# Kernel optimization log

Hardware: AMD Instinct MI355X
Metric: run time of the kernel (lower is better)

The kernel has to match this reference:

```python
import jax, jax.numpy as jnp
import numpy as np

N0, N1, N2, N3, B = 120000, 20000, 6000, 1600, 64
E1, E2, E3 = 480000, 144000, 38400
KS = 5  # kernel size per dim; K = 125 total


def spline_basis(pseudo, ks=KS):
    # open B-spline basis, degree 1, over [0,1]^3 (torch_spline_conv semantics)
    p = pseudo * (ks - 1)                       # (E,3)
    lo = jnp.clip(jnp.floor(p), 0.0, ks - 2.0)  # (E,3)
    f = p - lo                                  # fractional part
    bits = jnp.array([[(s >> d) & 1 for d in range(3)] for s in range(8)],
                     dtype=jnp.float32)         # (8,3) corner offsets
    w = jnp.where(bits[None] > 0, f[:, None, :], 1.0 - f[:, None, :])  # (E,8,3)
    basis = w[..., 0] * w[..., 1] * w[..., 2]   # (E,8)
    strides = jnp.array([1.0, ks, ks * ks], dtype=jnp.float32)
    kidx = ((lo[:, None, :] + bits[None]) * strides).sum(-1).astype(jnp.int32)  # (E,8)
    return basis, kidx


def spline_conv(x, edge_index, pseudo, W, root, bias, num_nodes):
    src, dst = edge_index[0], edge_index[1]
    basis, kidx = spline_basis(pseudo)                   # (E,8), (E,8)
    XW = jnp.einsum('ni,kio->nko', x, W)                 # (N,K,out)
    taps = XW[src[:, None], kidx]                        # (E,8,out) gather
    msg = (taps * basis[..., None]).sum(axis=1)          # (E,out)
    agg = jax.ops.segment_sum(msg, dst, num_segments=num_nodes)
    deg = jax.ops.segment_sum(jnp.ones_like(dst, jnp.float32), dst,
                              num_segments=num_nodes)
    agg = agg / jnp.maximum(deg, 1.0)[:, None]           # mean aggregation
    return agg + x @ root + bias


def seg_max(x, seg, n):
    v = jax.ops.segment_max(x, seg, num_segments=n)
    return jnp.where(jnp.isfinite(v), v, 0.0)  # empty voxels -> 0


def setup_inputs() -> dict:
    key = jax.random.key(0)
    ks = jax.random.split(key, 24)
    return {
        'x0': jax.random.uniform(ks[0], (N0, 1), jnp.float32),
        'cluster0': jax.random.randint(ks[1], (N0,), 0, N1),
        'edge1': jax.random.randint(ks[2], (2, E1), 0, N1),
        'pseudo1': jax.random.uniform(ks[3], (E1, 3), jnp.float32),
        'W1': jax.random.normal(ks[4], (125, 1, 64), jnp.float32) * 0.1,
        'root1': jax.random.normal(ks[5], (1, 64), jnp.float32) * 0.1,
        'b1': jnp.zeros((64,), jnp.float32),
        'cluster1': jax.random.randint(ks[6], (N1,), 0, N2),
        'edge2': jax.random.randint(ks[7], (2, E2), 0, N2),
        'pseudo2': jax.random.uniform(ks[8], (E2, 3), jnp.float32),
        'W2': jax.random.normal(ks[9], (125, 64, 64), jnp.float32) * 0.05,
        'root2': jax.random.normal(ks[10], (64, 64), jnp.float32) * 0.05,
        'b2': jnp.zeros((64,), jnp.float32),
        'cluster2': jax.random.randint(ks[11], (N2,), 0, N3),
        'edge3': jax.random.randint(ks[12], (2, E3), 0, N3),
        'pseudo3': jax.random.uniform(ks[13], (E3, 3), jnp.float32),
        'W3': jax.random.normal(ks[14], (125, 64, 128), jnp.float32) * 0.05,
        'root3': jax.random.normal(ks[15], (64, 128), jnp.float32) * 0.05,
        'b3': jnp.zeros((128,), jnp.float32),
        'cluster3': jax.random.randint(ks[16], (N3,), 0, B * 8),
        'fc1_w': jax.random.normal(ks[17], (1024, 256), jnp.float32) * 0.03,
        'fc1_b': jnp.zeros((256,), jnp.float32),
        'fc2_w': jax.random.normal(ks[18], (256, 10), jnp.float32) * 0.06,
        'fc2_b': jnp.zeros((10,), jnp.float32),
    }


def reference(x0, cluster0, edge1, pseudo1, W1, root1, b1,
              cluster1, edge2, pseudo2, W2, root2, b2,
              cluster2, edge3, pseudo3, W3, root3, b3,
              cluster3, fc1_w, fc1_b, fc2_w, fc2_b):
    x = seg_max(x0, cluster0, N1)                       # sparse voxel max pool 1
    x = jax.nn.elu(spline_conv(x, edge1, pseudo1, W1, root1, b1, N1))
    x = seg_max(x, cluster1, N2)                        # pool 2
    x = jax.nn.elu(spline_conv(x, edge2, pseudo2, W2, root2, b2, N2))
    x = seg_max(x, cluster2, N3)                        # pool 3
    x = jax.nn.elu(spline_conv(x, edge3, pseudo3, W3, root3, b3, N3))
    x = seg_max(x, cluster3, B * 8)                     # dense 2x2x2 voxel pool
    x = x.reshape(B, 8 * 128)
    x = jax.nn.elu(x @ fc1_w + fc1_b)
    x = x @ fc2_w + fc2_b
    return jax.nn.log_softmax(x, axis=1)
```

## Files before the change

kernel.cpp:

```cpp
#include <hip/hip_runtime.h>
#include <hip/hip_bf16.h>
#include <math.h>

#define N0c 120000
#define N1c 20000
#define N2c 6000
#define N3c 1600
#define E1c 480000
#define E2c 144000
#define E3c 38400

#define HB1 32
#define HB2 120
#define HB3 40
#define CVT2B 2000
#define CVT3B 4000
#define SS0B  469

typedef __attribute__((ext_vector_type(8))) short short8;
typedef __attribute__((ext_vector_type(4))) float f32x4;

__device__ __forceinline__ float eluf(float x) {
    return x > 0.0f ? x : expm1f(x);
}

__device__ __forceinline__ unsigned f2sort(float f) {
    unsigned u = __float_as_uint(f);
    return (u & 0x80000000u) ? ~u : (u | 0x80000000u);
}
__device__ __forceinline__ float sort2f(unsigned u) {
    unsigned bits = (u & 0x80000000u) ? (u & 0x7FFFFFFFu) : ~u;
    return __uint_as_float(bits);
}
__device__ __forceinline__ unsigned short f2bf(float v) {
    unsigned u = __float_as_uint(v);
    unsigned r = (u + 0x7FFFu + ((u >> 16) & 1u)) >> 16;
    return (unsigned short)r;
}

__global__ __launch_bounds__(256) void hist_all(
    const int* __restrict__ edge1, const int* __restrict__ edge2,
    const int* __restrict__ edge3,
    const float* __restrict__ pseudo2, const float* __restrict__ pseudo3,
    const float* __restrict__ W2, const float* __restrict__ W3,
    const float* __restrict__ x0, const int* __restrict__ cluster0,
    int* __restrict__ blockCnt1,
    int* __restrict__ blockCnt2, int* __restrict__ cntD2,
    int* __restrict__ blockCnt3, int* __restrict__ cntD3,
    unsigned short* __restrict__ W2t, unsigned short* __restrict__ W3t,
    unsigned* __restrict__ xm1)
{
    __shared__ int h[1250];
    int b = blockIdx.x, t = threadIdx.x;
    if (b < HB1) {
        for (int i = t; i < 1250; i += 256) h[i] = 0;
        __syncthreads();
        for (int e = b * 256 + t; e < E1c; e += HB1 * 256)
            atomicAdd(&h[edge1[E1c + e] >> 4], 1);
        __syncthreads();
        for (int i = t; i < 1250; i += 256) blockCnt1[i * HB1 + b] = h[i];
    } else if (b < HB1 + HB2 + HB3) {
        bool is2 = b < HB1 + HB2;
        int rb = is2 ? (b - HB1) : (b - HB1 - HB2);
        int nblk = is2 ? HB2 : HB3;
        int E = is2 ? E2c : E3c;
        const int* edge = is2 ? edge2 : edge3;
        const float* pseudo = is2 ? pseudo2 : pseudo3;
        int* blockCnt = is2 ? blockCnt2 : blockCnt3;
        int* dstCnt = is2 ? cntD2 : cntD3;
        int nb = is2 ? HB2 : HB3;
        if (t < 64) h[t] = 0;
        __syncthreads();
        for (int e = rb * 256 + t; e < E; e += nblk * 256) {
            int c = 0, mul = 1;
            #pragma unroll
            for (int d = 0; d < 3; d++) {
                float p = pseudo[e * 3 + d] * 4.0f;
                float l = fminf(fmaxf(floorf(p), 0.0f), 3.0f);
                c += (int)l * mul;
                mul <<= 2;
            }
            atomicAdd(&h[c], 1);
            atomicAdd(&dstCnt[edge[E + e]], 1);
        }
        __syncthreads();
        if (t < 64) blockCnt[t * nb + rb] = h[t];
    } else if (b < HB1 + HB2 + HB3 + CVT2B) {
        int idx = (b - (HB1 + HB2 + HB3)) * 256 + t;
        if (idx < 125 * 64 * 64) {
            int ic = idx & 63, kn = idx >> 6;
            int n = kn & 63, k = kn >> 6;
            W2t[idx] = f2bf(W2[((size_t)k * 64 + ic) * 64 + n]);
        }
    } else if (b < HB1 + HB2 + HB3 + CVT2B + CVT3B) {
        int idx = (b - (HB1 + HB2 + HB3 + CVT2B)) * 256 + t;
        if (idx < 125 * 128 * 64) {
            int ic = idx & 63, kn = idx >> 6;
            int n = kn & 127, k = kn >> 7;
            W3t[idx] = f2bf(W3[((size_t)k * 64 + ic) * 128 + n]);
        }
    } else {
        int idx = (b - (HB1 + HB2 + HB3 + CVT2B + CVT3B)) * 256 + t;
        if (idx < N0c)
            atomicMax(&xm1[cluster0[idx]], f2sort(x0[idx]));
    }
}

__global__ __launch_bounds__(256) void plan_tot(
    const int* __restrict__ blockCnt1, int* __restrict__ start1,
    const int* __restrict__ blockCnt2, int* __restrict__ binCnt2,
    int* __restrict__ binStart2, int* __restrict__ blkPrefix2,
    int* __restrict__ chunkBin2, int* __restrict__ chunkOff2,
    const int* __restrict__ blockCnt3, int* __restrict__ binCnt3,
    int* __restrict__ binStart3, int* __restrict__ blkPrefix3,
    int* __restrict__ chunkBin3, int* __restrict__ chunkOff3,
    const int* __restrict__ cntD2, int* __restrict__ dstStart2,
    const int* __restrict__ cntD3, int* __restrict__ dstStart3)
{
    __shared__ int ps[256];
    __shared__ int ps64[64];
    int t = threadIdx.x;

    int loc[5];
    int s = 0;
    #pragma unroll
    for (int i = 0; i < 5; i++) {
        int bin = t * 5 + i;
        int v = 0;
        if (bin < 1250) {
            const int4* row = (const int4*)(blockCnt1 + (size_t)bin * HB1);
            #pragma unroll
            for (int j = 0; j < HB1 / 4; j++) {
                int4 q = row[j];
                v += q.x + q.y + q.z + q.w;
            }
        }
        loc[i] = v;
        s += v;
    }
    ps[t] = s;
    __syncthreads();
    for (int ofs = 1; ofs < 256; ofs <<= 1) {
        int add = (t >= ofs) ? ps[t - ofs] : 0;
        __syncthreads();
        ps[t] += add;
        __syncthreads();
    }
    int run = (t == 0) ? 0 : ps[t - 1];
    #pragma unroll
    for (int i = 0; i < 5; i++) {
        int bin = t * 5 + i;
        if (bin < 1250) {
            start1[bin] = run;
            run += loc[i];
        }
    }
    if (t == 255) start1[1250] = run;
    __syncthreads();

    if (t < 64) {
        int v = 0;
        const int4* row = (const int4*)(blockCnt2 + (size_t)t * HB2);
        for (int j = 0; j < HB2 / 4; j++) {
            int4 q = row[j];
            v += q.x + q.y + q.z + q.w;
        }
        binCnt2[t] = v;
        ps64[t] = v;
    }
    __syncthreads();
    if (t == 0) {
        int s2 = 0, p = 0;
        for (int c = 0; c < 64; c++) {
            int v = ps64[c];
            binStart2[c] = s2;
            blkPrefix2[c] = p;
            s2 += v;
            p += (v + 63) >> 6;
        }
        binStart2[64] = s2;
        blkPrefix2[64] = p;
    }
    __syncthreads();
    if (t < 64) {
        int nch = (binCnt2[t] + 63) >> 6;
        int base = blkPrefix2[t];
        for (int j = 0; j < nch; j++) {
            chunkBin2[base + j] = t;
            chunkOff2[base + j] = j;
        }
    }
    __syncthreads();

    if (t < 64) {
        int v = 0;
        const int4* row = (const int4*)(blockCnt3 + (size_t)t * HB3);
        for (int j = 0; j < HB3 / 4; j++) {
            int4 q = row[j];
            v += q.x + q.y + q.z + q.w;
        }
        binCnt3[t] = v;
        ps64[t] = v;
    }
    __syncthreads();
    if (t == 0) {
        int s3 = 0, p = 0;
        for (int c = 0; c < 64; c++) {
            int v = ps64[c];
            binStart3[c] = s3;
            blkPrefix3[c] = p;
            s3 += v;
            p += (v + 63) >> 6;
        }
        binStart3[64] = s3;
        blkPrefix3[64] = p;
    }
    __syncthreads();
    if (t < 64) {
        int nch = (binCnt3[t] + 63) >> 6;
        int base = blkPrefix3[t];
        for (int j = 0; j < nch; j++) {
            chunkBin3[base + j] = t;
            chunkOff3[base + j] = j;
        }
    }
    __syncthreads();

    {
        int locd[24];
        int sd = 0;
        #pragma unroll
        for (int i = 0; i < 24; i++) {
            int bin = t * 24 + i;
            int vv = (bin < N2c) ? cntD2[bin] : 0;
            locd[i] = vv;
            sd += vv;
        }
        ps[t] = sd;
        __syncthreads();
        for (int ofs = 1; ofs < 256; ofs <<= 1) {
            int add = (t >= ofs) ? ps[t - ofs] : 0;
            __syncthreads();
            ps[t] += add;
            __syncthreads();
        }
        int rund = (t == 0) ? 0 : ps[t - 1];
        #pragma unroll
        for (int i = 0; i < 24; i++) {
            int bin = t * 24 + i;
            if (bin < N2c) { dstStart2[bin] = rund; rund += locd[i]; }
        }
        if (t == 255) dstStart2[N2c] = ps[255];
    }
    __syncthreads();

    {
        int locd[7];
        int sd = 0;
        #pragma unroll
        for (int i = 0; i < 7; i++) {
            int bin = t * 7 + i;
            int vv = (bin < N3c) ? cntD3[bin] : 0;
            locd[i] = vv;
            sd += vv;
        }
        ps[t] = sd;
        __syncthreads();
        for (int ofs = 1; ofs < 256; ofs <<= 1) {
            int add = (t >= ofs) ? ps[t - ofs] : 0;
            __syncthreads();
            ps[t] += add;
            __syncthreads();
        }
        int rund = (t == 0) ? 0 : ps[t - 1];
        #pragma unroll
        for (int i = 0; i < 7; i++) {
            int bin = t * 7 + i;
            if (bin < N3c) { dstStart3[bin] = rund; rund += locd[i]; }
        }
        if (t == 255) dstStart3[N3c] = ps[255];
    }
}

__global__ __launch_bounds__(256) void off_all(
    const int* __restrict__ blockCnt1, const int* __restrict__ start1,
    int* __restrict__ blockOff1,
    const int* __restrict__ blockCnt2, const int* __restrict__ binStart2,
    int* __restrict__ blockOff2,
    const int* __restrict__ blockCnt3, const int* __restrict__ binStart3,
    int* __restrict__ blockOff3)
{
    int r = blockIdx.x * 256 + threadIdx.x;
    if (r < 1250) {
        int run = start1[r];
        const int* c = blockCnt1 + (size_t)r * HB1;
        int* o = blockOff1 + (size_t)r * HB1;
        #pragma unroll 4
        for (int b = 0; b < HB1; b++) { o[b] = run; run += c[b]; }
    } else if (r < 1250 + 64) {
        int bin = r - 1250;
        int run = binStart2[bin];
        const int* c = blockCnt2 + (size_t)bin * HB2;
        int* o = blockOff2 + (size_t)bin * HB2;
        #pragma unroll 4
        for (int b = 0; b < HB2; b++) { o[b] = run; run += c[b]; }
    } else if (r < 1250 + 128) {
        int bin = r - 1314;
        int run = binStart3[bin];
        const int* c = blockCnt3 + (size_t)bin * HB3;
        int* o = blockOff3 + (size_t)bin * HB3;
        #pragma unroll 4
        for (int b = 0; b < HB3; b++) { o[b] = run; run += c[b]; }
    }
}

__global__ __launch_bounds__(256) void scatter_all(
    const int* __restrict__ edge1, const float* __restrict__ pseudo1,
    const int* __restrict__ edge2, const float* __restrict__ pseudo2,
    const int* __restrict__ edge3, const float* __restrict__ pseudo3,
    const int* __restrict__ blockOff1, const int* __restrict__ blockOff2,
    const int* __restrict__ blockOff3,
    int4* __restrict__ rec1, int4* __restrict__ rec2, int4* __restrict__ rec3,
    unsigned* __restrict__ xm1,
    const int* __restrict__ dstStart2, const int* __restrict__ dstStart3,
    int* __restrict__ curD2, int* __restrict__ curD3,
    int* __restrict__ posList2, int* __restrict__ posList3)
{
    __shared__ int cur[1250];
    int b = blockIdx.x, t = threadIdx.x;
    if (b < HB1) {
        for (int i = t; i < 1250; i += 256) cur[i] = blockOff1[(size_t)i * HB1 + b];
        __syncthreads();
        for (int e = b * 256 + t; e < E1c; e += HB1 * 256) {
            int src = edge1[e], dst = edge1[E1c + e];
            float f[3];
            int kbase = 0, mul5 = 1;
            #pragma unroll
            for (int d = 0; d < 3; d++) {
                float pp = pseudo1[e * 3 + d] * 4.0f;
                float l = fminf(fmaxf(floorf(pp), 0.0f), 3.0f);
                f[d] = pp - l;
                kbase += (int)l * mul5;
                mul5 *= 5;
            }
            int p = atomicAdd(&cur[dst >> 4], 1);
            rec1[p] = make_int4(src | ((dst & 15) << 16) | (kbase << 20),
                                __float_as_int(f[0]), __float_as_int(f[1]),
                                __float_as_int(f[2]));
        }
    } else if (b < HB1 + HB2 + HB3) {
        bool is2 = b < HB1 + HB2;
        int rb = is2 ? (b - HB1) : (b - HB1 - HB2);
        int nblk = is2 ? HB2 : HB3;
        int E = is2 ? E2c : E3c;
        const int* edge = is2 ? edge2 : edge3;
        const float* pseudo = is2 ? pseudo2 : pseudo3;
        const int* blockOff = is2 ? blockOff2 : blockOff3;
        int4* rec = is2 ? rec2 : rec3;
        const int* dstStart = is2 ? dstStart2 : dstStart3;
        int* curD = is2 ? curD2 : curD3;
        int* posList = is2 ? posList2 : posList3;
        int nb = is2 ? HB2 : HB3;
        if (t < 64) cur[t] = blockOff[(size_t)t * nb + rb];
        __syncthreads();
        for (int e = rb * 256 + t; e < E; e += nblk * 256) {
            int src = edge[e], dst = edge[E + e];
            float f[3];
            int c = 0, mul = 1;
            #pragma unroll
            for (int d = 0; d < 3; d++) {
                float pp = pseudo[e * 3 + d] * 4.0f;
                float l = fminf(fmaxf(floorf(pp), 0.0f), 3.0f);
                f[d] = pp - l;
                c += (int)l * mul;
                mul <<= 2;
            }
            int p = atomicAdd(&cur[c], 1);
            rec[p] = make_int4(src | (dst << 16),
                               __float_as_int(f[0]), __float_as_int(f[1]),
                               __float_as_int(f[2]));
            int qd = dstStart[dst] + atomicAdd(&curD[dst], 1);
            posList[qd] = p;
        }
    } else {
        int idx = (b - (HB1 + HB2 + HB3)) * 256 + t;
        if (idx < N1c) {
            float f = sort2f(xm1[idx]);
            unsigned bb = __float_as_uint(f);
            if ((bb & 0x7F800000u) == 0x7F800000u) f = 0.0f;
            ((float*)xm1)[idx] = f;
        }
    }
}

__global__ __launch_bounds__(256) void conv1_block(
    const int4* __restrict__ rec, const float* __restrict__ x,
    const int* __restrict__ start,
    const float* __restrict__ W, const float* __restrict__ root,
    const float* __restrict__ bias, const int* __restrict__ cl,
    unsigned* __restrict__ xmOut) {
    __shared__ float T[16][128];
    __shared__ int degL[16];
    int b = blockIdx.x;
    for (int j = threadIdx.x; j < 2048; j += 256) ((float*)T)[j] = 0.0f;
    if (threadIdx.x < 16) degL[threadIdx.x] = 0;
    __syncthreads();
    int s0 = start[b], s1 = start[b + 1];
    for (int i = s0 + threadIdx.x; i < s1; i += 256) {
        int4 r = rec[i];
        int src = r.x & 0xFFFF;
        int ln = (r.x >> 16) & 15;
        int kbase = r.x >> 20;
        float f0 = __int_as_float(r.y);
        float f1 = __int_as_float(r.z);
        float f2 = __int_as_float(r.w);
        float xv = x[src];
        #pragma unroll
        for (int s = 0; s < 8; s++) {
            int b0 = s & 1, b1 = (s >> 1) & 1, b2 = (s >> 2) & 1;
            float w0 = b0 ? f0 : 1.0f - f0;
            float w1 = b1 ? f1 : 1.0f - f1;
            float w2 = b2 ? f2 : 1.0f - f2;
            int k = kbase + b0 + 5 * b1 + 25 * b2;
            atomicAdd(&T[ln][k], xv * w0 * w1 * w2);
        }
        atomicAdd(&degL[ln], 1);
    }
    __syncthreads();
    int w = threadIdx.x >> 6, lane = threadIdx.x & 63;
    float acc[4] = {0.0f, 0.0f, 0.0f, 0.0f};
    for (int k = 0; k < 125; k++) {
        float wv = W[(k << 6) + lane];
        #pragma unroll
        for (int j = 0; j < 4; j++)
            acc[j] = fmaf(T[w + 4 * j][k], wv, acc[j]);
    }
    int v0 = b << 4;
    #pragma unroll
    for (int j = 0; j < 4; j++) {
        int ln = w + 4 * j;
        int v = v0 + ln;
        float d = fmaxf((float)degL[ln], 1.0f);
        float val = eluf(acc[j] / d + x[v] * root[lane] + bias[lane]);
        atomicMax(&xmOut[((size_t)cl[v] << 6) + lane], f2sort(val));
    }
}

__global__ void decode_cvt(unsigned* __restrict__ buf,
                           unsigned short* __restrict__ xb, int total) {
    int idx = blockIdx.x * blockDim.x + threadIdx.x;
    if (idx >= total) return;
    float f = sort2f(buf[idx]);
    unsigned b = __float_as_uint(f);
    if ((b & 0x7F800000u) == 0x7F800000u) f = 0.0f;
    ((float*)buf)[idx] = f;
    xb[idx] = f2bf(f);
}

__global__ void segmax_decode(unsigned* __restrict__ buf, int total) {
    int idx = blockIdx.x * blockDim.x + threadIdx.x;
    if (idx >= total) return;
    float f = sort2f(buf[idx]);
    unsigned b = __float_as_uint(f);
    if ((b & 0x7F800000u) == 0x7F800000u) f = 0.0f;
    ((float*)buf)[idx] = f;
}

template<int COUT>
__global__ __launch_bounds__(256) void spline_mfma(
    const int4* __restrict__ recs,
    const unsigned short* __restrict__ Wt,
    const unsigned short* __restrict__ xb,
    const int* __restrict__ binStart,
    const int* __restrict__ binCnt,
    const int* __restrict__ blkPrefix,
    const int* __restrict__ chunkBin,
    const int* __restrict__ chunkOff,
    float* __restrict__ msg)
{
    __shared__ float basisS[4][8][64];
    __shared__ int srcS[4][64];

    int w = threadIdx.x >> 6, lane = threadIdx.x & 63;
    int c = blockIdx.x * 4 + w;
    if (c >= blkPrefix[64]) return;
    int bin = chunkBin[c];
    int chunk = chunkOff[c];
    int cnt = binCnt[bin];

    {
        int pos = chunk * 64 + lane;
        bool act = pos < cnt;
        int4 r = act ? recs[binStart[bin] + pos] : make_int4(0, 0, 0, 0);
        srcS[w][lane] = r.x & 0xFFFF;
        float f0 = __int_as_float(r.y);
        float f1 = __int_as_float(r.z);
        float f2 = __int_as_float(r.w);
        #pragma unroll
        for (int s = 0; s < 8; s++) {
            float w0 = (s & 1) ? f0 : 1.0f - f0;
            float w1 = (s & 2) ? f1 : 1.0f - f1;
            float w2 = (s & 4) ? f2 : 1.0f - f2;
            basisS[w][s][lane] = act ? (w0 * w1 * w2) : 0.0f;
        }
    }
    __builtin_amdgcn_wave_barrier();
    __threadfence_block();

    int lo0 = bin & 3, lo1 = (bin >> 2) & 3, lo2 = bin >> 4;
    int kbase = lo0 + 5 * lo1 + 25 * lo2;
    int colOff = (COUT == 128) ? (blockIdx.y << 6) : 0;
    int q = lane >> 4;
    int mcol = lane & 15;

    short8 afr[4][2];
    #pragma unroll
    for (int rt = 0; rt < 4; rt++) {
        int src = srcS[w][rt * 16 + mcol];
        const unsigned short* xr = xb + ((size_t)src << 6) + q * 8;
        afr[rt][0] = *(const short8*)(xr);
        afr[rt][1] = *(const short8*)(xr + 32);
    }

    f32x4 acc[4][4];
    #pragma unroll
    for (int rt = 0; rt < 4; rt++)
        #pragma unroll
        for (int nt = 0; nt < 4; nt++)
            acc[rt][nt] = (f32x4){0.0f, 0.0f, 0.0f, 0.0f};
    const f32x4 zero4 = {0.0f, 0.0f, 0.0f, 0.0f};

    #pragma unroll 1
    for (int s = 0; s < 8; s++) {
        int k = kbase + (s & 1) + 5 * ((s >> 1) & 1) + 25 * (s >> 2);
        const unsigned short* Wk = Wt + ((size_t)k * COUT + colOff) * 64;
        short8 bfr[4][2];
        #pragma unroll
        for (int nt = 0; nt < 4; nt++) {
            const unsigned short* Wn = Wk + (size_t)(nt * 16 + mcol) * 64 + q * 8;
            bfr[nt][0] = *(const short8*)(Wn);
            bfr[nt][1] = *(const short8*)(Wn + 32);
        }
        #pragma unroll
        for (int rt = 0; rt < 4; rt++) {
            f32x4 ct[4];
            #pragma unroll
            for (int nt = 0; nt < 4; nt++) {
                ct[nt] = __builtin_amdgcn_mfma_f32_16x16x32_bf16(afr[rt][0], bfr[nt][0], zero4, 0, 0, 0);
                ct[nt] = __builtin_amdgcn_mfma_f32_16x16x32_bf16(afr[rt][1], bfr[nt][1], ct[nt], 0, 0, 0);
            }
            #pragma unroll
            for (int r = 0; r < 4; r++) {
                float bs = basisS[w][s][rt * 16 + q * 4 + r];
                #pragma unroll
                for (int nt = 0; nt < 4; nt++)
                    acc[rt][nt][r] = fmaf(bs, ct[nt][r], acc[rt][nt][r]);
            }
        }
    }

    int base = binStart[bin] + chunk * 64;
    #pragma unroll
    for (int rt = 0; rt < 4; rt++) {
        #pragma unroll
        for (int r = 0; r < 4; r++) {
            int row = rt * 16 + q * 4 + r;
            if (chunk * 64 + row < cnt) {
                float* mp = msg + (size_t)(base + row) * COUT + colOff + mcol;
                #pragma unroll
                for (int nt = 0; nt < 4; nt++)
                    mp[nt * 16] = acc[rt][nt][r];
            }
        }
    }
}

__global__ __launch_bounds__(256) void agg_update64(
    const float* __restrict__ msg, const int* __restrict__ posList,
    const int* __restrict__ dstStart,
    const float* __restrict__ xm, const float* __restrict__ root,
    const float* __restrict__ bias, const int* __restrict__ cl,
    unsigned* __restrict__ xmOut, int nNodes) {
    __shared__ float xsh[4][64];
    int w = threadIdx.x >> 6, lane = threadIdx.x & 63;
    int v = blockIdx.x * 4 + w;
    if (v >= nNodes) return;
    xsh[w][lane] = xm[((size_t)v << 6) + lane];
    int s0 = dstStart[v], s1 = dstStart[v + 1];
    float a0 = 0.0f, a1 = 0.0f, a2 = 0.0f, a3 = 0.0f;
    int i = s0;
    for (; i + 4 <= s1; i += 4) {
        int p0 = posList[i], p1 = posList[i + 1];
        int p2 = posList[i + 2], p3 = posList[i + 3];
        a0 += msg[((size_t)p0 << 6) + lane];
        a1 += msg[((size_t)p1 << 6) + lane];
        a2 += msg[((size_t)p2 << 6) + lane];
        a3 += msg[((size_t)p3 << 6) + lane];
    }
    for (; i < s1; i++)
        a0 += msg[((size_t)posList[i] << 6) + lane];
    float a = (a0 + a1 + a2 + a3) / fmaxf((float)(s1 - s0), 1.0f);
    float r = 0.0f;
    #pragma unroll 8
    for (int j = 0; j < 64; j++)
        r = fmaf(xsh[w][j], root[(j << 6) + lane], r);
    float val = eluf(a + r + bias[lane]);
    atomicMax(&xmOut[((size_t)cl[v] << 6) + lane], f2sort(val));
}

__global__ __launch_bounds__(256) void agg_update128(
    const float* __restrict__ msg, const int* __restrict__ posList,
    const int* __restrict__ dstStart,
    const float* __restrict__ xm, const float* __restrict__ root,
    const float* __restrict__ bias, const int* __restrict__ cl,
    unsigned* __restrict__ xmOut, int nNodes) {
    __shared__ float xsh[4][64];
    int w = threadIdx.x >> 6, lane = threadIdx.x & 63;
    int v = blockIdx.x * 4 + w;
    if (v >= nNodes) return;
    xsh[w][lane] = xm[((size_t)v << 6) + lane];
    int s0 = dstStart[v], s1 = dstStart[v + 1];
    float c0a = 0.0f, c0b = 0.0f, c1a = 0.0f, c1b = 0.0f;
    int i = s0;
    for (; i + 2 <= s1; i += 2) {
        int p0 = posList[i], p1 = posList[i + 1];
        const float* m0 = msg + ((size_t)p0 << 7);
        const float* m1 = msg + ((size_t)p1 << 7);
        c0a += m0[lane]; c0b += m0[64 + lane];
        c1a += m1[lane]; c1b += m1[64 + lane];
    }
    for (; i < s1; i++) {
        const float* m0 = msg + ((size_t)posList[i] << 7);
        c0a += m0[lane]; c0b += m0[64 + lane];
    }
    float dinv = 1.0f / fmaxf((float)(s1 - s0), 1.0f);
    float aa0 = (c0a + c1a) * dinv;
    float aa1 = (c0b + c1b) * dinv;
    float r0 = 0.0f, r1 = 0.0f;
    #pragma unroll 8
    for (int j = 0; j < 64; j++) {
        float xi = xsh[w][j];
        r0 = fmaf(xi, root[(j << 7) + lane], r0);
        r1 = fmaf(xi, root[(j << 7) + 64 + lane], r1);
    }
    unsigned* orow = xmOut + ((size_t)cl[v] << 7);
    atomicMax(&orow[lane], f2sort(eluf(aa0 + r0 + bias[lane])));
    atomicMax(&orow[64 + lane], f2sort(eluf(aa1 + r1 + bias[lane + 64])));
}

__global__ __launch_bounds__(256) void fc1_split(
    const float* __restrict__ xin, const float* __restrict__ w1,
    float* __restrict__ h) {
    __shared__ float xsh[128];
    int row = blockIdx.x, ks = blockIdx.y;
    int o = threadIdx.x;
    if (o < 128) xsh[o] = xin[row * 1024 + ks * 128 + o];
    __syncthreads();
    float acc = 0.0f;
    const float* wp = w1 + (size_t)ks * 128 * 256 + o;
    #pragma unroll 8
    for (int i = 0; i < 128; i++)
        acc = fmaf(xsh[i], wp[i * 256], acc);
    atomicAdd(&h[row * 256 + o], acc);
}

__global__ __launch_bounds__(64) void fc2_k(
    const float* __restrict__ h, const float* __restrict__ b1,
    const float* __restrict__ w2, const float* __restrict__ b2,
    float* __restrict__ out) {
    __shared__ float hs[256];
    __shared__ float lg[10];
    int row = blockIdx.x;
    int t = threadIdx.x;
    for (int i = t; i < 256; i += 64) hs[i] = eluf(h[row * 256 + i] + b1[i]);
    __syncthreads();
    if (t < 10) {
        float a = b2[t];
        for (int i = 0; i < 256; i++) a = fmaf(hs[i], w2[i * 10 + t], a);
        lg[t] = a;
    }
    __syncthreads();
    if (t < 10) {
        float m = -1e30f;
        #pragma unroll
        for (int j = 0; j < 10; j++) m = fmaxf(m, lg[j]);
        float sum = 0.0f;
        #pragma unroll
        for (int j = 0; j < 10; j++) sum += expf(lg[j] - m);
        out[row * 10 + t] = lg[t] - m - logf(sum);
    }
}

extern "C" void kernel_launch(void* const* d_in, const int* in_sizes, int n_in,
                              void* d_out, int out_size, void* d_ws, size_t ws_size,
                              hipStream_t stream) {
    const float* x0      = (const float*)d_in[0];
    const int*   cluster0= (const int*)d_in[1];
    const int*   edge1   = (const int*)d_in[2];
    const float* pseudo1 = (const float*)d_in[3];
    const float* W1      = (const float*)d_in[4];
    const float* root1   = (const float*)d_in[5];
    const float* b1      = (const float*)d_in[6];
    const int*   cluster1= (const int*)d_in[7];
    const int*   edge2   = (const int*)d_in[8];
    const float* pseudo2 = (const float*)d_in[9];
    const float* W2      = (const float*)d_in[10];
    const float* root2   = (const float*)d_in[11];
    const float* b2      = (const float*)d_in[12];
    const int*   cluster2= (const int*)d_in[13];
    const int*   edge3   = (const int*)d_in[14];
    const float* pseudo3 = (const float*)d_in[15];
    const float* W3      = (const float*)d_in[16];
    const float* root3   = (const float*)d_in[17];
    const float* b3      = (const float*)d_in[18];
    const int*   cluster3= (const int*)d_in[19];
    const float* fc1_w   = (const float*)d_in[20];
    const float* fc1_b   = (const float*)d_in[21];
    const float* fc2_w   = (const float*)d_in[22];
    const float* fc2_b   = (const float*)d_in[23];
    float* out = (float*)d_out;

    float* ws = (float*)d_ws;
    size_t off = 0;
    float* xm1  = ws + off; off += 20480;
    float* xm2  = ws + off; off += (size_t)N2c * 64;
    float* xm3  = ws + off; off += (size_t)N3c * 64;
    float* xm4  = ws + off; off += 512 * 128;
    float* h1   = ws + off; off += 64 * 256;
    int* cntD2   = (int*)(ws + off); off += 6016;
    int* cntD3   = (int*)(ws + off); off += 1664;
    int* curD2   = (int*)(ws + off); off += 6016;
    int* curD3   = (int*)(ws + off); off += 1664;
    size_t zeroFloats = off;
    int4* rec1 = (int4*)(ws + off); off += (size_t)E1c * 4;
    int4* rec2 = (int4*)(ws + off); off += (size_t)E2c * 4;
    int4* rec3 = (int4*)(ws + off); off += (size_t)E3c * 4;
    unsigned short* W2t = (unsigned short*)(ws + off); off += 256000;
    unsigned short* W3t = (unsigned short*)(ws + off); off += 512000;
    unsigned short* xb2 = (unsigned short*)(ws + off); off += 192000;
    unsigned short* xb3 = (unsigned short*)(ws + off); off += 51200;
    int* start1    = (int*)(ws + off); off += 1280;
    int* blockCnt1 = (int*)(ws + off); off += HB1 * 1250;
    int* blockOff1 = (int*)(ws + off); off += HB1 * 1250;
    int* blockCnt2 = (int*)(ws + off); off += HB2 * 64;
    int* blockOff2 = (int*)(ws + off); off += HB2 * 64;
    int* blockCnt3 = (int*)(ws + off); off += HB3 * 64;
    int* blockOff3 = (int*)(ws + off); off += HB3 * 64;
    int* binCnt2   = (int*)(ws + off); off += 64;
    int* binStart2 = (int*)(ws + off); off += 80;
    int* blkPrefix2= (int*)(ws + off); off += 80;
    int* chunkBin2 = (int*)(ws + off); off += 2560;
    int* chunkOff2 = (int*)(ws + off); off += 2560;
    int* binCnt3   = (int*)(ws + off); off += 64;
    int* binStart3 = (int*)(ws + off); off += 80;
    int* blkPrefix3= (int*)(ws + off); off += 80;
    int* chunkBin3 = (int*)(ws + off); off += 768;
    int* chunkOff3 = (int*)(ws + off); off += 768;
    int* dstStart2 = (int*)(ws + off); off += 6016;
    int* dstStart3 = (int*)(ws + off); off += 1664;
    int* posList2  = (int*)(ws + off); off += E2c;
    int* posList3  = (int*)(ws + off); off += E3c;
    float* msg = ws + off; off += (size_t)E2c * 64;

    hipMemsetAsync(d_ws, 0, zeroFloats * sizeof(float), stream);

    hist_all<<<HB1 + HB2 + HB3 + CVT2B + CVT3B + SS0B, 256, 0, stream>>>(
        edge1, edge2, edge3, pseudo2, pseudo3, W2, W3, x0, cluster0,
        blockCnt1, blockCnt2, cntD2, blockCnt3, cntD3,
        W2t, W3t, (unsigned*)xm1);

    plan_tot<<<1, 256, 0, stream>>>(
        blockCnt1, start1,
        blockCnt2, binCnt2, binStart2, blkPrefix2, chunkBin2, chunkOff2,
        blockCnt3, binCnt3, binStart3, blkPrefix3, chunkBin3, chunkOff3,
        cntD2, dstStart2, cntD3, dstStart3);

    off_all<<<6, 256, 0, stream>>>(
        blockCnt1, start1, blockOff1,
        blockCnt2, binStart2, blockOff2,
        blockCnt3, binStart3, blockOff3);

    scatter_all<<<HB1 + HB2 + HB3 + (N1c + 255) / 256, 256, 0, stream>>>(
        edge1, pseudo1, edge2, pseudo2, edge3, pseudo3,
        blockOff1, blockOff2, blockOff3, rec1, rec2, rec3, (unsigned*)xm1,
        dstStart2, dstStart3, curD2, curD3, posList2, posList3);

    conv1_block<<<1250, 256, 0, stream>>>(rec1, xm1, start1, W1, root1, b1,
                                          cluster1, (unsigned*)xm2);
    decode_cvt<<<(N2c * 64) / 256, 256, 0, stream>>>((unsigned*)xm2, xb2, N2c * 64);

    spline_mfma<64><<<dim3((E2c / 64 + 64 + 3) / 4, 1), 256, 0, stream>>>(
        rec2, W2t, xb2, binStart2, binCnt2, blkPrefix2, chunkBin2, chunkOff2, msg);
    agg_update64<<<(N2c + 3) / 4, 256, 0, stream>>>(msg, posList2, dstStart2,
                                                    xm2, root2, b2, cluster2,
                                                    (unsigned*)xm3, N2c);
    decode_cvt<<<(N3c * 64) / 256, 256, 0, stream>>>((unsigned*)xm3, xb3, N3c * 64);

    spline_mfma<128><<<dim3((E3c / 64 + 64 + 3) / 4, 2), 256, 0, stream>>>(
        rec3, W3t, xb3, binStart3, binCnt3, blkPrefix3, chunkBin3, chunkOff3, msg);
    agg_update128<<<(N3c + 3) / 4, 256, 0, stream>>>(msg, posList3, dstStart3,
                                                     xm3, root3, b3, cluster3,
                                                     (unsigned*)xm4, N3c);
    segmax_decode<<<(512 * 128) / 256, 256, 0, stream>>>((unsigned*)xm4, 512 * 128);

    fc1_split<<<dim3(64, 8), 256, 0, stream>>>(xm4, fc1_w, h1);
    fc2_k<<<64, 64, 0, stream>>>(h1, fc1_b, fc2_w, fc2_b, out);
}
```

Before: 349.9 us.

## Raise histogram block counts and accumulate bin totals atomically in hist_all

Histogram block counts for the three edge sets rise from 32/120/40 to 256/480/160 so the counting phase has more parallelism. Each block also atomically adds its per-bin counts into global bin totals, and the single-block planner reads those totals directly instead of summing per-block count rows. The cost is more global atomics, larger blockCnt/blockOff arrays, and more work for the per-block offset kernel (off_all), which still runs on only 6 blocks and now walks longer rows.

```diff
diff --git a/kernel.cpp b/kernel.cpp
--- a/kernel.cpp
+++ b/kernel.cpp
@@ -10,9 +10,9 @@
 #define E2c 144000
 #define E3c 38400
 
-#define HB1 32
-#define HB2 120
-#define HB3 40
+#define HB1 256
+#define HB2 480
+#define HB3 160
 #define CVT2B 2000
 #define CVT3B 4000
 #define SS0B  469
@@ -44,9 +44,9 @@
     const float* __restrict__ pseudo2, const float* __restrict__ pseudo3,
     const float* __restrict__ W2, const float* __restrict__ W3,
     const float* __restrict__ x0, const int* __restrict__ cluster0,
-    int* __restrict__ blockCnt1,
-    int* __restrict__ blockCnt2, int* __restrict__ cntD2,
-    int* __restrict__ blockCnt3, int* __restrict__ cntD3,
+    int* __restrict__ blockCnt1, int* __restrict__ binTot1,
+    int* __restrict__ blockCnt2, int* __restrict__ binTot2, int* __restrict__ cntD2,
+    int* __restrict__ blockCnt3, int* __restrict__ binTot3, int* __restrict__ cntD3,
     unsigned short* __restrict__ W2t, unsigned short* __restrict__ W3t,
     unsigned* __restrict__ xm1)
 {
@@ -58,7 +58,11 @@
         for (int e = b * 256 + t; e < E1c; e += HB1 * 256)
             atomicAdd(&h[edge1[E1c + e] >> 4], 1);
         __syncthreads();
-        for (int i = t; i < 1250; i += 256) blockCnt1[i * HB1 + b] = h[i];
+        for (int i = t; i < 1250; i += 256) {
+            int v = h[i];
+            blockCnt1[i * HB1 + b] = v;
+            if (v) atomicAdd(&binTot1[i], v);
+        }
     } else if (b < HB1 + HB2 + HB3) {
         bool is2 = b < HB1 + HB2;
         int rb = is2 ? (b - HB1) : (b - HB1 - HB2);
@@ -67,6 +71,7 @@
         const int* edge = is2 ? edge2 : edge3;
         const float* pseudo = is2 ? pseudo2 : pseudo3;
         int* blockCnt = is2 ? blockCnt2 : blockCnt3;
+        int* binTot = is2 ? binTot2 : binTot3;
         int* dstCnt = is2 ? cntD2 : cntD3;
         int nb = is2 ? HB2 : HB3;
         if (t < 64) h[t] = 0;
@@ -84,7 +89,11 @@
             atomicAdd(&dstCnt[edge[E + e]], 1);
         }
         __syncthreads();
-        if (t < 64) blockCnt[t * nb + rb] = h[t];
+        if (t < 64) {
+            int v = h[t];
+            blockCnt[t * nb + rb] = v;
+            if (v) atomicAdd(&binTot[t], v);
+        }
     } else if (b < HB1 + HB2 + HB3 + CVT2B) {
         int idx = (b - (HB1 + HB2 + HB3)) * 256 + t;
         if (idx < 125 * 64 * 64) {
@@ -107,11 +116,11 @@
 }
 
 __global__ __launch_bounds__(256) void plan_tot(
-    const int* __restrict__ blockCnt1, int* __restrict__ start1,
-    const int* __restrict__ blockCnt2, int* __restrict__ binCnt2,
+    const int* __restrict__ binTot1, int* __restrict__ start1,
+    const int* __restrict__ binTot2, int* __restrict__ binCnt2,
     int* __restrict__ binStart2, int* __restrict__ blkPrefix2,
     int* __restrict__ chunkBin2, int* __restrict__ chunkOff2,
-    const int* __restrict__ blockCnt3, int* __restrict__ binCnt3,
+    const int* __restrict__ binTot3, int* __restrict__ binCnt3,
     int* __restrict__ binStart3, int* __restrict__ blkPrefix3,
     int* __restrict__ chunkBin3, int* __restrict__ chunkOff3,
     const int* __restrict__ cntD2, int* __restrict__ dstStart2,
@@ -126,15 +135,7 @@
     #pragma unroll
     for (int i = 0; i < 5; i++) {
         int bin = t * 5 + i;
-        int v = 0;
-        if (bin < 1250) {
-            const int4* row = (const int4*)(blockCnt1 + (size_t)bin * HB1);
-            #pragma unroll
-            for (int j = 0; j < HB1 / 4; j++) {
-                int4 q = row[j];
-                v += q.x + q.y + q.z + q.w;
-            }
-        }
+        int v = (bin < 1250) ? binTot1[bin] : 0;
         loc[i] = v;
         s += v;
     }
@@ -159,12 +160,7 @@
     __syncthreads();
 
     if (t < 64) {
-        int v = 0;
-        const int4* row = (const int4*)(blockCnt2 + (size_t)t * HB2);
-        for (int j = 0; j < HB2 / 4; j++) {
-            int4 q = row[j];
-            v += q.x + q.y + q.z + q.w;
-        }
+        int v = binTot2[t];
         binCnt2[t] = v;
         ps64[t] = v;
     }
@@ -193,12 +189,7 @@
     __syncthreads();
 
     if (t < 64) {
-        int v = 0;
-        const int4* row = (const int4*)(blockCnt3 + (size_t)t * HB3);
-        for (int j = 0; j < HB3 / 4; j++) {
-            int4 q = row[j];
-            v += q.x + q.y + q.z + q.w;
-        }
+        int v = binTot3[t];
         binCnt3[t] = v;
         ps64[t] = v;
     }
@@ -731,6 +722,9 @@
     int* cntD3   = (int*)(ws + off); off += 1664;
     int* curD2   = (int*)(ws + off); off += 6016;
     int* curD3   = (int*)(ws + off); off += 1664;
+    int* binTot1 = (int*)(ws + off); off += 1280;
+    int* binTot2 = (int*)(ws + off); off += 64;
+    int* binTot3 = (int*)(ws + off); off += 64;
     size_t zeroFloats = off;
     int4* rec1 = (int4*)(ws + off); off += (size_t)E1c * 4;
     int4* rec2 = (int4*)(ws + off); off += (size_t)E2c * 4;
@@ -740,12 +734,12 @@
     unsigned short* xb2 = (unsigned short*)(ws + off); off += 192000;
     unsigned short* xb3 = (unsigned short*)(ws + off); off += 51200;
     int* start1    = (int*)(ws + off); off += 1280;
-    int* blockCnt1 = (int*)(ws + off); off += HB1 * 1250;
-    int* blockOff1 = (int*)(ws + off); off += HB1 * 1250;
-    int* blockCnt2 = (int*)(ws + off); off += HB2 * 64;
-    int* blockOff2 = (int*)(ws + off); off += HB2 * 64;
-    int* blockCnt3 = (int*)(ws + off); off += HB3 * 64;
-    int* blockOff3 = (int*)(ws + off); off += HB3 * 64;
+    int* blockCnt1 = (int*)(ws + off); off += (size_t)HB1 * 1250;
+    int* blockOff1 = (int*)(ws + off); off += (size_t)HB1 * 1250;
+    int* blockCnt2 = (int*)(ws + off); off += (size_t)HB2 * 64;
+    int* blockOff2 = (int*)(ws + off); off += (size_t)HB2 * 64;
+    int* blockCnt3 = (int*)(ws + off); off += (size_t)HB3 * 64;
+    int* blockOff3 = (int*)(ws + off); off += (size_t)HB3 * 64;
     int* binCnt2   = (int*)(ws + off); off += 64;
     int* binStart2 = (int*)(ws + off); off += 80;
     int* blkPrefix2= (int*)(ws + off); off += 80;
@@ -766,13 +760,13 @@
 
     hist_all<<<HB1 + HB2 + HB3 + CVT2B + CVT3B + SS0B, 256, 0, stream>>>(
         edge1, edge2, edge3, pseudo2, pseudo3, W2, W3, x0, cluster0,
-        blockCnt1, blockCnt2, cntD2, blockCnt3, cntD3,
-        W2t, W3t, (unsigned*)xm1);
+        blockCnt1, binTot1, blockCnt2, binTot2, cntD2,
+        blockCnt3, binTot3, cntD3, W2t, W3t, (unsigned*)xm1);
 
     plan_tot<<<1, 256, 0, stream>>>(
-        blockCnt1, start1,
-        blockCnt2, binCnt2, binStart2, blkPrefix2, chunkBin2, chunkOff2,
-        blockCnt3, binCnt3, binStart3, blkPrefix3, chunkBin3, chunkOff3,
+        binTot1, start1,
+        binTot2, binCnt2, binStart2, blkPrefix2, chunkBin2, chunkOff2,
+        binTot3, binCnt3, binStart3, blkPrefix3, chunkBin3, chunkOff3,
         cntD2, dstStart2, cntD3, dstStart3);
 
     off_all<<<6, 256, 0, stream>>>(
```

Result: slower. 363.7 us (+3.9%).
